# Optimization experiments

Hardware: AMD Instinct MI355X
Metric: run time of the kernel (lower is better)

## Reference

```python
import jax, jax.numpy as jnp
import numpy as np

D_MODEL = 1024
B, T = 4, 2048
NEG = -1000000000.0


def setup_inputs() -> dict:
    key = jax.random.key(0)
    kq, kk, kv = jax.random.split(key, 3)
    query = jax.random.normal(kq, (B, T, D_MODEL), dtype=jnp.float32)
    k = jax.random.normal(kk, (B, T, D_MODEL), dtype=jnp.float32)
    value = jax.random.normal(kv, (B, T, D_MODEL), dtype=jnp.float32)
    # causal mask: 1.0 where attention is disallowed (strictly upper triangular)
    mask = jnp.triu(jnp.ones((T, T), dtype=jnp.float32), k=1)
    return {"query": query, "key": k, "value": value, "mask": mask}


def reference(query, key, value, mask):
    # dk = sqrt(1/d_model); logits = QK^T / dk  (i.e. * sqrt(d_model)) -- faithful to source
    dk = jnp.sqrt(jnp.float32(1.0) / jnp.float32(D_MODEL))
    attn_logits = jnp.einsum("btc,bsc->bts", query, key) / dk
    attn_logits = attn_logits + mask * NEG  # mask broadcasts over batch
    score = jax.nn.softmax(attn_logits, axis=-1)
    attention = jnp.einsum("bts,bsc->btc", score, value)
    return attention
```

## Files before the change

kernel.cpp:

```cpp
#include <hip/hip_runtime.h>

#define BB 4
#define TT 2048
#define DD 1024
#define SCALE 32.0f
#define NTILE 136
#define L2E 1.4426950408889634f

typedef _Float16 f16;
typedef __attribute__((ext_vector_type(4))) _Float16 half4v;
typedef __attribute__((ext_vector_type(8))) _Float16 half8v;
typedef __attribute__((ext_vector_type(16))) float f32x16;

typedef const __attribute__((address_space(1))) unsigned int* gas_u32;
typedef __attribute__((address_space(3))) unsigned int* las_u32;

static __device__ inline void gload16(const void* g, void* l) {
    __builtin_amdgcn_global_load_lds((gas_u32)g, (las_u32)l, 16, 0, 0);
}

static __device__ inline half8v ld_frag(const f16* p) {
    half4v a = *(const half4v*)p;
    half4v b = *(const half4v*)(p + 4);
    half8v r;
    r[0] = a[0]; r[1] = a[1]; r[2] = a[2]; r[3] = a[3];
    r[4] = b[0]; r[5] = b[1]; r[6] = b[2]; r[7] = b[3];
    return r;
}


__global__ __launch_bounds__(256) void repack_qk(const float* __restrict__ Q,
                                                 const float* __restrict__ K,
                                                 f16* __restrict__ Qt,
                                                 f16* __restrict__ Kt) {
    __shared__ char rl[32768];
    int bid = blockIdx.x;
    int which = bid >> 10, b = (bid >> 8) & 3, mi = (bid >> 4) & 15, ks4 = bid & 15;
    const float* src = which ? K : Q;
    f16* dst = which ? Kt : Qt;
    float sc = which ? 1.0f : SCALE;

    int tid = threadIdx.x;
    int r = tid >> 1, h = tid & 1;
    const float* p = src + ((size_t)(b * TT + mi * 128 + r)) * DD + ks4 * 64 + h * 32;
#pragma unroll
    for (int j = 0; j < 4; ++j) {
        float4 x0 = *(const float4*)(p + j * 8);
        float4 x1 = *(const float4*)(p + j * 8 + 4);
        float vv[8] = {x0.x, x0.y, x0.z, x0.w, x1.x, x1.y, x1.z, x1.w};
        half8v hi, lo;
#pragma unroll
        for (int e = 0; e < 8; ++e) {
            float x = vv[e] * sc;
            f16 hh = (f16)x;
            hi[e] = hh;
            lo[e] = (f16)(x - (float)hh);
        }
        int ckl = h * 2 + (j >> 1);
        int shalf = j & 1;
        *(half8v*)(rl + ckl * 8192 + shalf * 2048 + r * 16) = hi;
        *(half8v*)(rl + ckl * 8192 + (2 + shalf) * 2048 + r * 16) = lo;
    }
    __syncthreads();
    char* gout = (char*)dst + ((size_t)((b * 16 + mi) * 64 + ks4 * 4)) * 8192 + tid * 128;
#pragma unroll
    for (int q = 0; q < 8; ++q)
        *(float4*)(gout + q * 16) = *(float4*)(rl + tid * 128 + q * 16);
}

__global__ __launch_bounds__(256) void transpose_v(const float* __restrict__ V,
                                                   f16* __restrict__ Vt) {
    __shared__ float Vs[64][129];
    int bid = blockIdx.x;
    int b = bid >> 8, kb = (bid >> 3) & 31, nj = bid & 7;
    const float* src = V + ((size_t)(b * TT + kb * 64)) * DD + nj * 128;
    int tid = threadIdx.x;
#pragma unroll
    for (int it = 0; it < 8; ++it) {
        int f4 = it * 256 + tid;
        int row = f4 >> 5, c4 = f4 & 31;
        float4 x = *(const float4*)(src + (size_t)row * DD + c4 * 4);
        Vs[row][c4 * 4 + 0] = x.x;
        Vs[row][c4 * 4 + 1] = x.y;
        Vs[row][c4 * 4 + 2] = x.z;
        Vs[row][c4 * 4 + 3] = x.w;
    }
    __syncthreads();
#pragma unroll
    for (int qq = 0; qq < 4; ++qq) {
        int q = tid * 4 + qq;
        int ckl = q >> 9, s = (q >> 7) & 3, n = q & 127;
        half8v hv;
#pragma unroll
        for (int e = 0; e < 8; ++e) hv[e] = (f16)Vs[ckl * 32 + s * 8 + e][n];
        char* out = (char*)Vt + ((size_t)((b * 8 + nj) * 64 + kb * 2 + ckl)) * 8192
                    + s * 2048 + n * 16;
        *(half8v*)out = hv;
    }
}

__global__ __launch_bounds__(256, 3) void k1_qk5(const f16* __restrict__ Qt,
                                                 const f16* __restrict__ Kt,
                                                 float* __restrict__ S) {
    __shared__ char lds[49152];

    int bid0 = blockIdx.x;
    int bid = (bid0 & 7) * (BB * NTILE / 8) + (bid0 >> 3);
    int b = bid / NTILE, rr0 = bid % NTILE;
    int mi = 0;
    while ((mi + 1) * (mi + 2) / 2 <= rr0) ++mi;
    int nj = rr0 - mi * (mi + 1) / 2;

    const char* Abase = (const char*)Qt + ((size_t)((b * 16 + mi) * 64)) * 8192;
    const char* Bbase = (const char*)Kt + ((size_t)((b * 16 + nj) * 64)) * 8192;
    float* Sb = S + (size_t)b * TT * TT + (size_t)(mi * 128) * TT + nj * 128;

    int tid = threadIdx.x;
    int lane = tid & 63;
    int wv = tid >> 6;
    int l31 = lane & 31, lhi = lane >> 5;
    int wrow = wv >> 1, wcol = wv & 1;

    int aoff[2], boff[2];
#pragma unroll
    for (int f = 0; f < 2; ++f) {
        aoff[f] = lhi * 2048 + (wrow * 64 + f * 32 + l31) * 16;
        boff[f] = lhi * 2048 + (wcol * 64 + f * 32 + l31) * 16;
    }
    int lane_go = wv * 2048 + lane * 16;
    int lane_lo = wv * 2048;

    f32x16 acc[2][2] = {};

#define K1_STAGE(CK, BUF)                                                       \
    {                                                                           \
        const char* ga = Abase + (size_t)(CK) * 8192 + lane_go;                 \
        const char* gb = Bbase + (size_t)(CK) * 8192 + lane_go;                 \
        char* la = lds + (BUF) * 16384 + lane_lo;                               \
        char* lb = la + 8192;                                                   \
        gload16(ga, la);                                                        \
        gload16(ga + 1024, la + 1024);                                          \
        gload16(gb, lb);                                                        \
        gload16(gb + 1024, lb + 1024);                                          \
    }

    K1_STAGE(0, 0);
    K1_STAGE(1, 1);
    int cb = 0;
    int sb = 2;
    for (int ck = 0; ck < 64; ++ck) {
        if (ck < 63) asm volatile("s_waitcnt vmcnt(4)" ::: "memory");
        else         asm volatile("s_waitcnt vmcnt(0)" ::: "memory");
        __builtin_amdgcn_s_barrier();
        if (ck + 2 < 64) K1_STAGE(ck + 2, sb);
        const char* As = lds + cb * 16384;
        const char* Bs = As + 8192;
        half8v ah[2], al[2], bh[2], bl[2];
#pragma unroll
        for (int f = 0; f < 2; ++f) {
            ah[f] = *(const half8v*)(As + aoff[f]);
            al[f] = *(const half8v*)(As + aoff[f] + 4096);
            bh[f] = *(const half8v*)(Bs + boff[f]);
            bl[f] = *(const half8v*)(Bs + boff[f] + 4096);
        }
#pragma unroll
        for (int fm = 0; fm < 2; ++fm)
#pragma unroll
            for (int fn = 0; fn < 2; ++fn) {
                acc[fm][fn] = __builtin_amdgcn_mfma_f32_32x32x16_f16(ah[fm], bh[fn], acc[fm][fn], 0, 0, 0);
                acc[fm][fn] = __builtin_amdgcn_mfma_f32_32x32x16_f16(ah[fm], bl[fn], acc[fm][fn], 0, 0, 0);
                acc[fm][fn] = __builtin_amdgcn_mfma_f32_32x32x16_f16(al[fm], bh[fn], acc[fm][fn], 0, 0, 0);
            }
        cb = (cb == 2) ? 0 : cb + 1;
        sb = (sb == 2) ? 0 : sb + 1;
    }
#undef K1_STAGE
#pragma unroll
    for (int fm = 0; fm < 2; ++fm)
#pragma unroll
        for (int fn = 0; fn < 2; ++fn)
#pragma unroll
            for (int g = 0; g < 16; ++g) {
                int rr = (g & 3) + 8 * (g >> 2) + 4 * lhi;
                int row = wrow * 64 + fm * 32 + rr;
                int col = wcol * 64 + fn * 32 + l31;
                Sb[(size_t)row * TT + col] = acc[fm][fn][g];
            }
}

__global__ __launch_bounds__(256) void k1b3(const float* __restrict__ S,
                                            f16* __restrict__ Pt) {
    __shared__ float red[4];
    int rowid = blockIdx.x;
    int b = rowid >> 11, t = rowid & (TT - 1);
    const float* Sr = S + ((size_t)b * TT + t) * TT;
    int tid = threadIdx.x;
    int nv = t + 1;
    int mi = t >> 7, r = t & 127;
    int rowend = (mi + 1) << 7;
    int c = tid * 8;
    bool act = c < rowend;

    float v[8] = {0, 0, 0, 0, 0, 0, 0, 0};
    if (act) {
        float4 x0 = *(const float4*)(Sr + c);
        float4 x1 = *(const float4*)(Sr + c + 4);
        v[0] = x0.x; v[1] = x0.y; v[2] = x0.z; v[3] = x0.w;
        v[4] = x1.x; v[5] = x1.y; v[6] = x1.z; v[7] = x1.w;
    }

    float m = -3.0e38f;
    if (act) {
#pragma unroll
        for (int j = 0; j < 8; ++j)
            if (c + j < nv) m = fmaxf(m, v[j]);
    }
#pragma unroll
    for (int o = 32; o > 0; o >>= 1) m = fmaxf(m, __shfl_xor(m, o));
    if ((tid & 63) == 0) red[tid >> 6] = m;
    __syncthreads();
    m = fmaxf(fmaxf(red[0], red[1]), fmaxf(red[2], red[3]));
    __syncthreads();

    float e[8];
    float s = 0.f;
#pragma unroll
    for (int j = 0; j < 8; ++j) {
        e[j] = (act && c + j < nv) ? exp2f((v[j] - m) * L2E) : 0.0f;
        s += e[j];
    }
#pragma unroll
    for (int o = 32; o > 0; o >>= 1) s += __shfl_xor(s, o);
    if ((tid & 63) == 0) red[tid >> 6] = s;
    __syncthreads();
    s = red[0] + red[1] + red[2] + red[3];
    float inv = 1.0f / s;

    if (act) {
        half8v hv;
#pragma unroll
        for (int j = 0; j < 8; ++j) hv[j] = (f16)(e[j] * inv);
        int ck = c >> 5, sl = (c >> 3) & 3;
        char* dst = (char*)Pt + ((size_t)((b * 16 + mi) * 64 + ck)) * 8192
                    + sl * 2048 + r * 16;
        *(half8v*)dst = hv;
    }
}

__global__ __launch_bounds__(256, 3) void k2_pv5(const f16* __restrict__ Pt,
                                                 const f16* __restrict__ Vt,
                                                 float* __restrict__ O) {
    __shared__ char lds[49152];

    int bid0 = blockIdx.x;
    int bid = (bid0 & 7) * 64 + (bid0 >> 3);
    int b = bid >> 7, mi = (bid >> 3) & 15, nj = bid & 7;
    int kch = (mi + 1) * 4;

    const char* Abase = (const char*)Pt + ((size_t)((b * 16 + mi) * 64)) * 8192;
    const char* Bbase = (const char*)Vt + ((size_t)((b * 8 + nj) * 64)) * 8192;
    float* Ob = O + (size_t)b * TT * DD + (size_t)(mi * 128) * DD + nj * 128;

    int tid = threadIdx.x;
    int lane = tid & 63;
    int wv = tid >> 6;
    int l31 = lane & 31, lhi = lane >> 5;
    int wrow = wv >> 1, wcol = wv & 1;

    int arow[2], brow[2];
#pragma unroll
    for (int f = 0; f < 2; ++f) {
        arow[f] = (wrow * 64 + f * 32 + l31) * 16;
        brow[f] = (wcol * 64 + f * 32 + l31) * 16;
    }
    int lane_go = wv * 2048 + lane * 16;
    int lane_lo = wv * 2048;

    f32x16 acc[2][2] = {};

#define K2_STAGE(CK, BUF)                                                       \
    {                                                                           \
        const char* ga = Abase + (size_t)(CK) * 8192 + lane_go;                 \
        const char* gb = Bbase + (size_t)(CK) * 8192 + lane_go;                 \
        char* la = lds + (BUF) * 16384 + lane_lo;                               \
        char* lb = la + 8192;                                                   \
        gload16(ga, la);                                                        \
        gload16(ga + 1024, la + 1024);                                          \
        gload16(gb, lb);                                                        \
        gload16(gb + 1024, lb + 1024);                                          \
    }

    K2_STAGE(0, 0);
    K2_STAGE(1, 1);
    int cb = 0, sb = 2;
    for (int it = 0; it < kch; ++it) {
        if (it + 1 < kch) asm volatile("s_waitcnt vmcnt(4)" ::: "memory");
        else              asm volatile("s_waitcnt vmcnt(0)" ::: "memory");
        __builtin_amdgcn_s_barrier();
        if (it + 2 < kch) K2_STAGE(it + 2, sb);
        const char* As = lds + cb * 16384;
        const char* Bs = As + 8192;
#pragma unroll
        for (int ks = 0; ks < 2; ++ks) {
            int slot = (ks * 2 + lhi) * 2048;
            half8v a0 = *(const half8v*)(As + slot + arow[0]);
            half8v a1 = *(const half8v*)(As + slot + arow[1]);
            half8v b0 = *(const half8v*)(Bs + slot + brow[0]);
            half8v b1 = *(const half8v*)(Bs + slot + brow[1]);
            acc[0][0] = __builtin_amdgcn_mfma_f32_32x32x16_f16(a0, b0, acc[0][0], 0, 0, 0);
            acc[0][1] = __builtin_amdgcn_mfma_f32_32x32x16_f16(a0, b1, acc[0][1], 0, 0, 0);
            acc[1][0] = __builtin_amdgcn_mfma_f32_32x32x16_f16(a1, b0, acc[1][0], 0, 0, 0);
            acc[1][1] = __builtin_amdgcn_mfma_f32_32x32x16_f16(a1, b1, acc[1][1], 0, 0, 0);
        }
        cb = (cb == 2) ? 0 : cb + 1;
        sb = (sb == 2) ? 0 : sb + 1;
    }
#undef K2_STAGE
#pragma unroll
    for (int fm = 0; fm < 2; ++fm)
#pragma unroll
        for (int fn = 0; fn < 2; ++fn)
#pragma unroll
            for (int g = 0; g < 16; ++g) {
                int rr = (g & 3) + 8 * (g >> 2) + 4 * lhi;
                int row = wrow * 64 + fm * 32 + rr;
                int col = wcol * 64 + fn * 32 + l31;
                Ob[(size_t)row * DD + col] = acc[fm][fn][g];
            }
}

__global__ __launch_bounds__(256, 2) void k1_qk(const float* __restrict__ Q,
                                                const float* __restrict__ Kmat,
                                                float* __restrict__ S) {
    __shared__ f16 Ah[128][36], Al[128][36], Bh[128][36], Bl[128][36];
    int bid = blockIdx.x;
    int b = bid / NTILE, r = bid % NTILE;
    int mi = 0;
    while ((mi + 1) * (mi + 2) / 2 <= r) ++mi;
    int nj = r - mi * (mi + 1) / 2;
    const float* Qb = Q + ((size_t)b * TT + (size_t)mi * 128) * DD;
    const float* Kb = Kmat + ((size_t)b * TT + (size_t)nj * 128) * DD;
    float* Sb = S + (size_t)b * TT * TT + (size_t)(mi * 128) * TT + nj * 128;
    int tid = threadIdx.x;
    int lane = tid & 63;
    int wave = tid >> 6;
    int l31 = lane & 31, lhi = lane >> 5;
    int wrow = wave >> 1, wcol = wave & 1;
    int r0 = tid >> 1;
    int c0 = (tid & 1) * 16;
    f32x16 acc[2][2] = {};
    float4 abuf[4], bbuf[4];
#pragma unroll
    for (int j = 0; j < 4; ++j) {
        abuf[j] = *(const float4*)(Qb + (size_t)r0 * DD + c0 + 4 * j);
        bbuf[j] = *(const float4*)(Kb + (size_t)r0 * DD + c0 + 4 * j);
    }
    for (int ch = 0; ch < DD / 32; ++ch) {
        __syncthreads();
#pragma unroll
        for (int j = 0; j < 4; ++j) {
            float4 a = abuf[j], bq = bbuf[j];
            float ax[4] = {a.x * SCALE, a.y * SCALE, a.z * SCALE, a.w * SCALE};
            float bx[4] = {bq.x, bq.y, bq.z, bq.w};
            half4v ahv, alv, bhv, blv;
#pragma unroll
            for (int e = 0; e < 4; ++e) {
                f16 h = (f16)ax[e];
                ahv[e] = h;
                alv[e] = (f16)(ax[e] - (float)h);
                f16 g = (f16)bx[e];
                bhv[e] = g;
                blv[e] = (f16)(bx[e] - (float)g);
            }
            *(half4v*)&Ah[r0][c0 + 4 * j] = ahv;
            *(half4v*)&Al[r0][c0 + 4 * j] = alv;
            *(half4v*)&Bh[r0][c0 + 4 * j] = bhv;
            *(half4v*)&Bl[r0][c0 + 4 * j] = blv;
        }
        __syncthreads();
// ... 165 lines not shown
    const float* q = Q + ((size_t)b * TT + t) * DD;
    int tid = threadIdx.x;
    for (int j = tid; j < DD; j += 256) { qs[j] = q[j] * SCALE; osum[j] = 0.f; }
    __syncthreads();
    float m = -3.0e38f, l = 0.f;
    for (int s = 0; s <= t; ++s) {
        const float* kr = Kmat + ((size_t)b * TT + s) * DD;
        float part = 0.f;
#pragma unroll
        for (int j = 0; j < 4; ++j) part += qs[tid * 4 + j] * kr[tid * 4 + j];
#pragma unroll
        for (int o = 32; o > 0; o >>= 1) part += __shfl_xor(part, o);
        if ((tid & 63) == 0) red[tid >> 6] = part;
        __syncthreads();
        float dot = red[0] + red[1] + red[2] + red[3];
        float mn = fmaxf(m, dot);
        float f = exp2f((m - mn) * 1.44269504f);
        float e = exp2f((dot - mn) * 1.44269504f);
        l = l * f + e;
        const float* vr = V + ((size_t)b * TT + s) * DD;
#pragma unroll
        for (int j = 0; j < 4; ++j) {
            int c = tid * 4 + j;
            osum[c] = osum[c] * f + e * vr[c];
        }
        m = mn;
        __syncthreads();
    }
    float inv = 1.f / l;
    for (int j = tid; j < DD; j += 256) O[((size_t)b * TT + t) * DD + j] = osum[j] * inv;
}

extern "C" void kernel_launch(void* const* d_in, const int* in_sizes, int n_in,
                              void* d_out, int out_size, void* d_ws, size_t ws_size,
                              hipStream_t stream) {
    const float* Q = (const float*)d_in[0];
    const float* K = (const float*)d_in[1];
    const float* V = (const float*)d_in[2];
    float* O = (float*)d_out;

    const size_t MB = 1024 * 1024;
    const size_t QT_B = 32 * MB, KT_B = 32 * MB, VT_B = 16 * MB, S_B = 64 * MB;
    const size_t FULL = QT_B + KT_B + VT_B + S_B;

    size_t sbytes = (size_t)BB * TT * TT * 4;
    size_t pbytes = (size_t)BB * TT * TT * 2;

    if (ws_size >= FULL) {
        f16* Qt = (f16*)d_ws;
        f16* Kt = (f16*)((char*)d_ws + QT_B);
        f16* Vt = (f16*)((char*)d_ws + QT_B + KT_B);
        float* S = (float*)((char*)d_ws + QT_B + KT_B + VT_B);
        f16* Pt = (f16*)d_ws;
        hipLaunchKernelGGL(repack_qk, dim3(2048), dim3(256), 0, stream, Q, K, Qt, Kt);
        hipLaunchKernelGGL(transpose_v, dim3(1024), dim3(256), 0, stream, V, Vt);
        hipLaunchKernelGGL(k1_qk5, dim3(BB * NTILE), dim3(256), 0, stream, Qt, Kt, S);
        hipLaunchKernelGGL(k1b3, dim3(BB * TT), dim3(256), 0, stream, S, Pt);
        hipLaunchKernelGGL(k2_pv5, dim3(512), dim3(256), 0, stream, Pt, Vt, O);
    } else if (ws_size >= sbytes + pbytes) {
        float* S = (float*)d_ws;
        f16* P = (f16*)((char*)d_ws + sbytes);
        hipLaunchKernelGGL(k1_qk, dim3(BB * NTILE), dim3(256), 0, stream, Q, K, S);
        hipLaunchKernelGGL(k1b_softmax, dim3(BB * TT), dim3(256), 0, stream, S, P);
        hipLaunchKernelGGL(k2_pv, dim3(BB * 16 * 8), dim3(256), 0, stream, P, V, O);
    } else {
        hipLaunchKernelGGL(fa_fallback, dim3(BB * TT), dim3(256), 0, stream, Q, K, V, O);
    }
}
```

Before: 164.1 us.

## Use two waves per block with 64x128 per-wave tiles in QK and PV GEMMs

Both MFMA GEMM kernels now run 128 threads (2 waves) instead of 256 (4 waves). Each wave computes a 64x128 output tile instead of 64x64. One wave stages the A tile and the other the B tile through global_load_lds. This gives more MFMA work per LDS fragment load and fewer LDS reads per flop. In exchange it doubles accumulator registers, halves the waves per CU available to hide latency, and keeps the same 48KB LDS per block, which caps occupancy.

```diff
diff --git a/kernel.cpp b/kernel.cpp
--- a/kernel.cpp
+++ b/kernel.cpp
@@ -99,7 +99,7 @@
     }
 }
 
-__global__ __launch_bounds__(256, 3) void k1_qk5(const f16* __restrict__ Qt,
+__global__ __launch_bounds__(128, 2) void k1_qk6(const f16* __restrict__ Qt,
                                                  const f16* __restrict__ Kt,
                                                  float* __restrict__ S) {
     __shared__ char lds[49152];
@@ -119,54 +119,53 @@
     int lane = tid & 63;
     int wv = tid >> 6;
     int l31 = lane & 31, lhi = lane >> 5;
-    int wrow = wv >> 1, wcol = wv & 1;
-
-    int aoff[2], boff[2];
-#pragma unroll
-    for (int f = 0; f < 2; ++f) {
-        aoff[f] = lhi * 2048 + (wrow * 64 + f * 32 + l31) * 16;
-        boff[f] = lhi * 2048 + (wcol * 64 + f * 32 + l31) * 16;
-    }
-    int lane_go = wv * 2048 + lane * 16;
-    int lane_lo = wv * 2048;
-
-    f32x16 acc[2][2] = {};
+
+    int aoff[2], boff[4];
+#pragma unroll
+    for (int f = 0; f < 2; ++f)
+        aoff[f] = lhi * 2048 + (wv * 64 + f * 32 + l31) * 16;
+#pragma unroll
+    for (int n = 0; n < 4; ++n)
+        boff[n] = lhi * 2048 + (n * 32 + l31) * 16;
+
+    int lane_go = lane * 16;
+    const char* gsrcbase = wv ? Bbase : Abase;
+
+    f32x16 acc[2][4] = {};
 
 #define K1_STAGE(CK, BUF)                                                       \
     {                                                                           \
-        const char* ga = Abase + (size_t)(CK) * 8192 + lane_go;                 \
-        const char* gb = Bbase + (size_t)(CK) * 8192 + lane_go;                 \
-        char* la = lds + (BUF) * 16384 + lane_lo;                               \
-        char* lb = la + 8192;                                                   \
-        gload16(ga, la);                                                        \
-        gload16(ga + 1024, la + 1024);                                          \
-        gload16(gb, lb);                                                        \
-        gload16(gb + 1024, lb + 1024);                                          \
+        const char* gs = gsrcbase + (size_t)(CK) * 8192 + lane_go;              \
+        char* ld = lds + (BUF) * 16384 + wv * 8192;                             \
+        _Pragma("unroll") for (int i = 0; i < 8; ++i)                           \
+            gload16(gs + i * 1024, ld + i * 1024);                              \
     }
 
     K1_STAGE(0, 0);
     K1_STAGE(1, 1);
-    int cb = 0;
-    int sb = 2;
+    int cb = 0, sb = 2;
     for (int ck = 0; ck < 64; ++ck) {
-        if (ck < 63) asm volatile("s_waitcnt vmcnt(4)" ::: "memory");
+        if (ck < 63) asm volatile("s_waitcnt vmcnt(8)" ::: "memory");
         else         asm volatile("s_waitcnt vmcnt(0)" ::: "memory");
         __builtin_amdgcn_s_barrier();
         if (ck + 2 < 64) K1_STAGE(ck + 2, sb);
         const char* As = lds + cb * 16384;
         const char* Bs = As + 8192;
-        half8v ah[2], al[2], bh[2], bl[2];
+        half8v ah[2], al[2], bh[4], bl[4];
 #pragma unroll
         for (int f = 0; f < 2; ++f) {
             ah[f] = *(const half8v*)(As + aoff[f]);
             al[f] = *(const half8v*)(As + aoff[f] + 4096);
-            bh[f] = *(const half8v*)(Bs + boff[f]);
-            bl[f] = *(const half8v*)(Bs + boff[f] + 4096);
+        }
+#pragma unroll
+        for (int n = 0; n < 4; ++n) {
+            bh[n] = *(const half8v*)(Bs + boff[n]);
+            bl[n] = *(const half8v*)(Bs + boff[n] + 4096);
         }
 #pragma unroll
         for (int fm = 0; fm < 2; ++fm)
 #pragma unroll
-            for (int fn = 0; fn < 2; ++fn) {
+            for (int fn = 0; fn < 4; ++fn) {
                 acc[fm][fn] = __builtin_amdgcn_mfma_f32_32x32x16_f16(ah[fm], bh[fn], acc[fm][fn], 0, 0, 0);
                 acc[fm][fn] = __builtin_amdgcn_mfma_f32_32x32x16_f16(ah[fm], bl[fn], acc[fm][fn], 0, 0, 0);
                 acc[fm][fn] = __builtin_amdgcn_mfma_f32_32x32x16_f16(al[fm], bh[fn], acc[fm][fn], 0, 0, 0);
@@ -178,12 +177,12 @@
 #pragma unroll
     for (int fm = 0; fm < 2; ++fm)
 #pragma unroll
-        for (int fn = 0; fn < 2; ++fn)
+        for (int fn = 0; fn < 4; ++fn)
 #pragma unroll
             for (int g = 0; g < 16; ++g) {
                 int rr = (g & 3) + 8 * (g >> 2) + 4 * lhi;
-                int row = wrow * 64 + fm * 32 + rr;
-                int col = wcol * 64 + fn * 32 + l31;
+                int row = wv * 64 + fm * 32 + rr;
+                int col = fn * 32 + l31;
                 Sb[(size_t)row * TT + col] = acc[fm][fn][g];
             }
 }
@@ -247,7 +246,7 @@
     }
 }
 
-__global__ __launch_bounds__(256, 3) void k2_pv5(const f16* __restrict__ Pt,
+__global__ __launch_bounds__(128, 2) void k2_pv6(const f16* __restrict__ Pt,
                                                  const f16* __restrict__ Vt,
                                                  float* __restrict__ O) {
     __shared__ char lds[49152];
@@ -265,36 +264,31 @@
     int lane = tid & 63;
     int wv = tid >> 6;
     int l31 = lane & 31, lhi = lane >> 5;
-    int wrow = wv >> 1, wcol = wv & 1;
-
-    int arow[2], brow[2];
-#pragma unroll
-    for (int f = 0; f < 2; ++f) {
-        arow[f] = (wrow * 64 + f * 32 + l31) * 16;
-        brow[f] = (wcol * 64 + f * 32 + l31) * 16;
-    }
-    int lane_go = wv * 2048 + lane * 16;
-    int lane_lo = wv * 2048;
-
-    f32x16 acc[2][2] = {};
+
+    int arow[2], brow[4];
+#pragma unroll
+    for (int f = 0; f < 2; ++f) arow[f] = (wv * 64 + f * 32 + l31) * 16;
+#pragma unroll
+    for (int n = 0; n < 4; ++n) brow[n] = (n * 32 + l31) * 16;
+
+    int lane_go = lane * 16;
+    const char* gsrcbase = wv ? Bbase : Abase;
+
+    f32x16 acc[2][4] = {};
 
 #define K2_STAGE(CK, BUF)                                                       \
     {                                                                           \
-        const char* ga = Abase + (size_t)(CK) * 8192 + lane_go;                 \
-        const char* gb = Bbase + (size_t)(CK) * 8192 + lane_go;                 \
-        char* la = lds + (BUF) * 16384 + lane_lo;                               \
-        char* lb = la + 8192;                                                   \
-        gload16(ga, la);                                                        \
-        gload16(ga + 1024, la + 1024);                                          \
-        gload16(gb, lb);                                                        \
-        gload16(gb + 1024, lb + 1024);                                          \
+        const char* gs = gsrcbase + (size_t)(CK) * 8192 + lane_go;              \
+        char* ld = lds + (BUF) * 16384 + wv * 8192;                             \
+        _Pragma("unroll") for (int i = 0; i < 8; ++i)                           \
+            gload16(gs + i * 1024, ld + i * 1024);                              \
     }
 
     K2_STAGE(0, 0);
     K2_STAGE(1, 1);
     int cb = 0, sb = 2;
     for (int it = 0; it < kch; ++it) {
-        if (it + 1 < kch) asm volatile("s_waitcnt vmcnt(4)" ::: "memory");
+        if (it + 1 < kch) asm volatile("s_waitcnt vmcnt(8)" ::: "memory");
         else              asm volatile("s_waitcnt vmcnt(0)" ::: "memory");
         __builtin_amdgcn_s_barrier();
         if (it + 2 < kch) K2_STAGE(it + 2, sb);
@@ -307,10 +301,16 @@
             half8v a1 = *(const half8v*)(As + slot + arow[1]);
             half8v b0 = *(const half8v*)(Bs + slot + brow[0]);
             half8v b1 = *(const half8v*)(Bs + slot + brow[1]);
+            half8v b2 = *(const half8v*)(Bs + slot + brow[2]);
+            half8v b3 = *(const half8v*)(Bs + slot + brow[3]);
             acc[0][0] = __builtin_amdgcn_mfma_f32_32x32x16_f16(a0, b0, acc[0][0], 0, 0, 0);
             acc[0][1] = __builtin_amdgcn_mfma_f32_32x32x16_f16(a0, b1, acc[0][1], 0, 0, 0);
+            acc[0][2] = __builtin_amdgcn_mfma_f32_32x32x16_f16(a0, b2, acc[0][2], 0, 0, 0);
+            acc[0][3] = __builtin_amdgcn_mfma_f32_32x32x16_f16(a0, b3, acc[0][3], 0, 0, 0);
             acc[1][0] = __builtin_amdgcn_mfma_f32_32x32x16_f16(a1, b0, acc[1][0], 0, 0, 0);
             acc[1][1] = __builtin_amdgcn_mfma_f32_32x32x16_f16(a1, b1, acc[1][1], 0, 0, 0);
+            acc[1][2] = __builtin_amdgcn_mfma_f32_32x32x16_f16(a1, b2, acc[1][2], 0, 0, 0);
+            acc[1][3] = __builtin_amdgcn_mfma_f32_32x32x16_f16(a1, b3, acc[1][3], 0, 0, 0);
         }
         cb = (cb == 2) ? 0 : cb + 1;
         sb = (sb == 2) ? 0 : sb + 1;
@@ -319,12 +319,12 @@
 #pragma unroll
     for (int fm = 0; fm < 2; ++fm)
 #pragma unroll
-        for (int fn = 0; fn < 2; ++fn)
+        for (int fn = 0; fn < 4; ++fn)
 #pragma unroll
             for (int g = 0; g < 16; ++g) {
                 int rr = (g & 3) + 8 * (g >> 2) + 4 * lhi;
-                int row = wrow * 64 + fm * 32 + rr;
-                int col = wcol * 64 + fn * 32 + l31;
+                int row = wv * 64 + fm * 32 + rr;
+                int col = fn * 32 + l31;
                 Ob[(size_t)row * DD + col] = acc[fm][fn][g];
             }
 }
@@ -598,9 +598,9 @@
         f16* Pt = (f16*)d_ws;
         hipLaunchKernelGGL(repack_qk, dim3(2048), dim3(256), 0, stream, Q, K, Qt, Kt);
         hipLaunchKernelGGL(transpose_v, dim3(1024), dim3(256), 0, stream, V, Vt);
-        hipLaunchKernelGGL(k1_qk5, dim3(BB * NTILE), dim3(256), 0, stream, Qt, Kt, S);
+        hipLaunchKernelGGL(k1_qk6, dim3(BB * NTILE), dim3(128), 0, stream, Qt, Kt, S);
         hipLaunchKernelGGL(k1b3, dim3(BB * TT), dim3(256), 0, stream, S, Pt);
-        hipLaunchKernelGGL(k2_pv5, dim3(512), dim3(256), 0, stream, Pt, Vt, O);
+        hipLaunchKernelGGL(k2_pv6, dim3(512), dim3(128), 0, stream, Pt, Vt, O);
     } else if (ws_size >= sbytes + pbytes) {
         float* S = (float*)d_ws;
         f16* P = (f16*)((char*)d_ws + sbytes);
```

New measurement: 179.1 us. 1.09x slower.

## Merge Q/K/V prep kernels and halve QK/PV tiles to 64x128 for more blocks

Applied to the files above, without the earlier changes.

Merges the Q/K repack and the V transpose into one prep kernel to save a launch. The QK^T and PV GEMM kernels now use 64x128 output tiles computed by 2 waves of 128 threads, with a new mapping over the causal tiles, instead of 128x128 tiles on 4 waves. This doubles the grid (1088 and 1024 blocks versus 544 and 512) for better CU coverage and finer causal load balance. In exchange, each K/V tile is loaded from memory twice as often, MFMA work per byte loaded is lower, and the LDS footprint per block changes.

```diff
diff --git a/kernel.cpp b/kernel.cpp
--- a/kernel.cpp
+++ b/kernel.cpp
@@ -29,137 +29,149 @@
 }
 
 
-__global__ __launch_bounds__(256) void repack_qk(const float* __restrict__ Q,
-                                                 const float* __restrict__ K,
-                                                 f16* __restrict__ Qt,
-                                                 f16* __restrict__ Kt) {
-    __shared__ char rl[32768];
+__global__ __launch_bounds__(256) void prep(const float* __restrict__ Q,
+                                            const float* __restrict__ K,
+                                            const float* __restrict__ V,
+                                            f16* __restrict__ Qt,
+                                            f16* __restrict__ Kt,
+                                            f16* __restrict__ Vt) {
+    __shared__ char plds[33024];
     int bid = blockIdx.x;
-    int which = bid >> 10, b = (bid >> 8) & 3, mi = (bid >> 4) & 15, ks4 = bid & 15;
-    const float* src = which ? K : Q;
-    f16* dst = which ? Kt : Qt;
-    float sc = which ? 1.0f : SCALE;
-
-    int tid = threadIdx.x;
-    int r = tid >> 1, h = tid & 1;
-    const float* p = src + ((size_t)(b * TT + mi * 128 + r)) * DD + ks4 * 64 + h * 32;
-#pragma unroll
-    for (int j = 0; j < 4; ++j) {
-        float4 x0 = *(const float4*)(p + j * 8);
-        float4 x1 = *(const float4*)(p + j * 8 + 4);
-        float vv[8] = {x0.x, x0.y, x0.z, x0.w, x1.x, x1.y, x1.z, x1.w};
-        half8v hi, lo;
-#pragma unroll
-        for (int e = 0; e < 8; ++e) {
-            float x = vv[e] * sc;
-            f16 hh = (f16)x;
-            hi[e] = hh;
-            lo[e] = (f16)(x - (float)hh);
-        }
-        int ckl = h * 2 + (j >> 1);
-        int shalf = j & 1;
-        *(half8v*)(rl + ckl * 8192 + shalf * 2048 + r * 16) = hi;
-        *(half8v*)(rl + ckl * 8192 + (2 + shalf) * 2048 + r * 16) = lo;
-    }
-    __syncthreads();
-    char* gout = (char*)dst + ((size_t)((b * 16 + mi) * 64 + ks4 * 4)) * 8192 + tid * 128;
-#pragma unroll
-    for (int q = 0; q < 8; ++q)
-        *(float4*)(gout + q * 16) = *(float4*)(rl + tid * 128 + q * 16);
-}
-
-__global__ __launch_bounds__(256) void transpose_v(const float* __restrict__ V,
-                                                   f16* __restrict__ Vt) {
-    __shared__ float Vs[64][129];
-    int bid = blockIdx.x;
-    int b = bid >> 8, kb = (bid >> 3) & 31, nj = bid & 7;
-    const float* src = V + ((size_t)(b * TT + kb * 64)) * DD + nj * 128;
-    int tid = threadIdx.x;
-#pragma unroll
-    for (int it = 0; it < 8; ++it) {
-        int f4 = it * 256 + tid;
-        int row = f4 >> 5, c4 = f4 & 31;
-        float4 x = *(const float4*)(src + (size_t)row * DD + c4 * 4);
-        Vs[row][c4 * 4 + 0] = x.x;
-        Vs[row][c4 * 4 + 1] = x.y;
-        Vs[row][c4 * 4 + 2] = x.z;
-        Vs[row][c4 * 4 + 3] = x.w;
-    }
-    __syncthreads();
-#pragma unroll
-    for (int qq = 0; qq < 4; ++qq) {
-        int q = tid * 4 + qq;
-        int ckl = q >> 9, s = (q >> 7) & 3, n = q & 127;
-        half8v hv;
-#pragma unroll
-        for (int e = 0; e < 8; ++e) hv[e] = (f16)Vs[ckl * 32 + s * 8 + e][n];
-        char* out = (char*)Vt + ((size_t)((b * 8 + nj) * 64 + kb * 2 + ckl)) * 8192
-                    + s * 2048 + n * 16;
-        *(half8v*)out = hv;
-    }
-}
-
-__global__ __launch_bounds__(256, 3) void k1_qk5(const f16* __restrict__ Qt,
+    int tid = threadIdx.x;
+    if (bid < 2048) {
+        char* rl = plds;
+        int which = bid >> 10, b = (bid >> 8) & 3, mi = (bid >> 4) & 15, ks4 = bid & 15;
+        const float* src = which ? K : Q;
+        f16* dst = which ? Kt : Qt;
+        float sc = which ? 1.0f : SCALE;
+        int r = tid >> 1, h = tid & 1;
+        const float* p = src + ((size_t)(b * TT + mi * 128 + r)) * DD + ks4 * 64 + h * 32;
+#pragma unroll
+        for (int j = 0; j < 4; ++j) {
+            float4 x0 = *(const float4*)(p + j * 8);
+            float4 x1 = *(const float4*)(p + j * 8 + 4);
+            float vv[8] = {x0.x, x0.y, x0.z, x0.w, x1.x, x1.y, x1.z, x1.w};
+            half8v hi, lo;
+#pragma unroll
+            for (int e = 0; e < 8; ++e) {
+                float x = vv[e] * sc;
+                f16 hh = (f16)x;
+                hi[e] = hh;
+                lo[e] = (f16)(x - (float)hh);
+            }
+            int ckl = h * 2 + (j >> 1);
+            int shalf = j & 1;
+            *(half8v*)(rl + ckl * 8192 + shalf * 2048 + r * 16) = hi;
+            *(half8v*)(rl + ckl * 8192 + (2 + shalf) * 2048 + r * 16) = lo;
+        }
+        __syncthreads();
+        char* gout = (char*)dst + ((size_t)((b * 16 + mi) * 64 + ks4 * 4)) * 8192 + tid * 128;
+#pragma unroll
+        for (int q = 0; q < 8; ++q)
+            *(float4*)(gout + q * 16) = *(float4*)(rl + tid * 128 + q * 16);
+    } else {
+        float (*Vs)[129] = (float(*)[129])plds;
+        int bid2 = bid - 2048;
+        int b = bid2 >> 8, kb = (bid2 >> 3) & 31, nj = bid2 & 7;
+        const float* src = V + ((size_t)(b * TT + kb * 64)) * DD + nj * 128;
+#pragma unroll
+        for (int it = 0; it < 8; ++it) {
+            int f4 = it * 256 + tid;
+            int row = f4 >> 5, c4 = f4 & 31;
+            float4 x = *(const float4*)(src + (size_t)row * DD + c4 * 4);
+            Vs[row][c4 * 4 + 0] = x.x;
+            Vs[row][c4 * 4 + 1] = x.y;
+            Vs[row][c4 * 4 + 2] = x.z;
+            Vs[row][c4 * 4 + 3] = x.w;
+        }
+        __syncthreads();
+#pragma unroll
+        for (int qq = 0; qq < 4; ++qq) {
+            int q = tid * 4 + qq;
+            int ckl = q >> 9, s = (q >> 7) & 3, n = q & 127;
+            half8v hv;
+#pragma unroll
+            for (int e = 0; e < 8; ++e) hv[e] = (f16)Vs[ckl * 32 + s * 8 + e][n];
+            char* out = (char*)Vt + ((size_t)((b * 8 + nj) * 64 + kb * 2 + ckl)) * 8192
+                        + s * 2048 + n * 16;
+            *(half8v*)out = hv;
+        }
+    }
+}
+
+__global__ __launch_bounds__(128, 2) void k1_qk7(const f16* __restrict__ Qt,
                                                  const f16* __restrict__ Kt,
                                                  float* __restrict__ S) {
-    __shared__ char lds[49152];
+    __shared__ char lds[36864];
 
     int bid0 = blockIdx.x;
-    int bid = (bid0 & 7) * (BB * NTILE / 8) + (bid0 >> 3);
-    int b = bid / NTILE, rr0 = bid % NTILE;
-    int mi = 0;
-    while ((mi + 1) * (mi + 2) / 2 <= rr0) ++mi;
-    int nj = rr0 - mi * (mi + 1) / 2;
-
-    const char* Abase = (const char*)Qt + ((size_t)((b * 16 + mi) * 64)) * 8192;
+    int bid = (bid0 & 7) * 136 + (bid0 >> 3);
+    int b = bid / 272, r = bid % 272;
+    int p = 0;
+    while ((p + 1) * (p + 2) <= r) ++p;
+    int rem = r - p * (p + 1);
+    int second = (rem >= p + 1);
+    int mi2 = 2 * p + second;
+    int nj = second ? rem - (p + 1) : rem;
+    int mi = mi2 >> 1, rhalf = mi2 & 1;
+
+    const char* Abase = (const char*)Qt + ((size_t)((b * 16 + mi) * 64)) * 8192
+                        + rhalf * 1024;
     const char* Bbase = (const char*)Kt + ((size_t)((b * 16 + nj) * 64)) * 8192;
-    float* Sb = S + (size_t)b * TT * TT + (size_t)(mi * 128) * TT + nj * 128;
+    float* Sb = S + (size_t)b * TT * TT + (size_t)(mi2 * 64) * TT + nj * 128;
 
     int tid = threadIdx.x;
     int lane = tid & 63;
     int wv = tid >> 6;
     int l31 = lane & 31, lhi = lane >> 5;
-    int wrow = wv >> 1, wcol = wv & 1;
 
     int aoff[2], boff[2];
 #pragma unroll
     for (int f = 0; f < 2; ++f) {
-        aoff[f] = lhi * 2048 + (wrow * 64 + f * 32 + l31) * 16;
-        boff[f] = lhi * 2048 + (wcol * 64 + f * 32 + l31) * 16;
-    }
-    int lane_go = wv * 2048 + lane * 16;
-    int lane_lo = wv * 2048;
+        aoff[f] = lhi * 1024 + (f * 32 + l31) * 16;
+        boff[f] = lhi * 2048 + (wv * 64 + f * 32 + l31) * 16;
+    }
+    int lane16 = lane * 16;
 
     f32x16 acc[2][2] = {};
 
 #define K1_STAGE(CK, BUF)                                                       \
     {                                                                           \
-        const char* ga = Abase + (size_t)(CK) * 8192 + lane_go;                 \
-        const char* gb = Bbase + (size_t)(CK) * 8192 + lane_go;                 \
-        char* la = lds + (BUF) * 16384 + lane_lo;                               \
-        char* lb = la + 8192;                                                   \
-        gload16(ga, la);                                                        \
-        gload16(ga + 1024, la + 1024);                                          \
-        gload16(gb, lb);                                                        \
-        gload16(gb + 1024, lb + 1024);                                          \
+        const char* ga = Abase + (size_t)(CK) * 8192 + lane16;                  \
+        const char* gb = Bbase + (size_t)(CK) * 8192 + lane16;                  \
+        char* l0 = lds + (BUF) * 12288;                                         \
+        if (wv == 0) {                                                          \
+            gload16(ga, l0);                                                    \
+            gload16(ga + 2048, l0 + 1024);                                      \
+            gload16(ga + 4096, l0 + 2048);                                      \
+            gload16(ga + 6144, l0 + 3072);                                      \
+            gload16(gb, l0 + 4096);                                             \
+            gload16(gb + 1024, l0 + 5120);                                      \
+        } else {                                                                \
+            gload16(gb + 2048, l0 + 6144);                                      \
+            gload16(gb + 3072, l0 + 7168);                                      \
+            gload16(gb + 4096, l0 + 8192);                                      \
+            gload16(gb + 5120, l0 + 9216);                                      \
+            gload16(gb + 6144, l0 + 10240);                                     \
+            gload16(gb + 7168, l0 + 11264);                                     \
+        }                                                                       \
     }
 
     K1_STAGE(0, 0);
     K1_STAGE(1, 1);
-    int cb = 0;
-    int sb = 2;
+    int cb = 0, sb = 2;
     for (int ck = 0; ck < 64; ++ck) {
-        if (ck < 63) asm volatile("s_waitcnt vmcnt(4)" ::: "memory");
+        if (ck < 63) asm volatile("s_waitcnt vmcnt(6)" ::: "memory");
         else         asm volatile("s_waitcnt vmcnt(0)" ::: "memory");
         __builtin_amdgcn_s_barrier();
         if (ck + 2 < 64) K1_STAGE(ck + 2, sb);
-        const char* As = lds + cb * 16384;
-        const char* Bs = As + 8192;
+        const char* As = lds + cb * 12288;
+        const char* Bs = As + 4096;
         half8v ah[2], al[2], bh[2], bl[2];
 #pragma unroll
         for (int f = 0; f < 2; ++f) {
             ah[f] = *(const half8v*)(As + aoff[f]);
-            al[f] = *(const half8v*)(As + aoff[f] + 4096);
+            al[f] = *(const half8v*)(As + aoff[f] + 2048);
             bh[f] = *(const half8v*)(Bs + boff[f]);
             bl[f] = *(const half8v*)(Bs + boff[f] + 4096);
         }
@@ -182,8 +194,8 @@
 #pragma unroll
             for (int g = 0; g < 16; ++g) {
                 int rr = (g & 3) + 8 * (g >> 2) + 4 * lhi;
-                int row = wrow * 64 + fm * 32 + rr;
-                int col = wcol * 64 + fn * 32 + l31;
+                int row = fm * 32 + rr;
+                int col = wv * 64 + fn * 32 + l31;
                 Sb[(size_t)row * TT + col] = acc[fm][fn][g];
             }
 }
@@ -247,66 +259,77 @@
     }
 }
 
-__global__ __launch_bounds__(256, 3) void k2_pv5(const f16* __restrict__ Pt,
+__global__ __launch_bounds__(128, 2) void k2_pv7(const f16* __restrict__ Pt,
                                                  const f16* __restrict__ Vt,
                                                  float* __restrict__ O) {
-    __shared__ char lds[49152];
+    __shared__ char lds[36864];
 
     int bid0 = blockIdx.x;
-    int bid = (bid0 & 7) * 64 + (bid0 >> 3);
-    int b = bid >> 7, mi = (bid >> 3) & 15, nj = bid & 7;
-    int kch = (mi + 1) * 4;
-
-    const char* Abase = (const char*)Pt + ((size_t)((b * 16 + mi) * 64)) * 8192;
+    int bid = (bid0 & 7) * 128 + (bid0 >> 3);
+    int b = bid >> 8, r = (bid >> 3) & 31, nj = bid & 7;
+    int kch = 2 * r + 2;
+    int mi = r >> 1, rhalf = r & 1;
+
+    const char* Abase = (const char*)Pt + ((size_t)((b * 16 + mi) * 64)) * 8192
+                        + rhalf * 1024;
     const char* Bbase = (const char*)Vt + ((size_t)((b * 8 + nj) * 64)) * 8192;
-    float* Ob = O + (size_t)b * TT * DD + (size_t)(mi * 128) * DD + nj * 128;
+    float* Ob = O + (size_t)b * TT * DD + (size_t)(r * 64) * DD + nj * 128;
 
     int tid = threadIdx.x;
     int lane = tid & 63;
     int wv = tid >> 6;
     int l31 = lane & 31, lhi = lane >> 5;
-    int wrow = wv >> 1, wcol = wv & 1;
+    int lane16 = lane * 16;
 
     int arow[2], brow[2];
 #pragma unroll
     for (int f = 0; f < 2; ++f) {
-        arow[f] = (wrow * 64 + f * 32 + l31) * 16;
-        brow[f] = (wcol * 64 + f * 32 + l31) * 16;
-    }
-    int lane_go = wv * 2048 + lane * 16;
-    int lane_lo = wv * 2048;
+        arow[f] = (f * 32 + l31) * 16;
+        brow[f] = (wv * 64 + f * 32 + l31) * 16;
+    }
 
     f32x16 acc[2][2] = {};
 
 #define K2_STAGE(CK, BUF)                                                       \
     {                                                                           \
-        const char* ga = Abase + (size_t)(CK) * 8192 + lane_go;                 \
-        const char* gb = Bbase + (size_t)(CK) * 8192 + lane_go;                 \
-        char* la = lds + (BUF) * 16384 + lane_lo;                               \
-        char* lb = la + 8192;                                                   \
-        gload16(ga, la);                                                        \
-        gload16(ga + 1024, la + 1024);                                          \
-        gload16(gb, lb);                                                        \
-        gload16(gb + 1024, lb + 1024);                                          \
+        const char* ga = Abase + (size_t)(CK) * 8192 + lane16;                  \
+        const char* gb = Bbase + (size_t)(CK) * 8192 + lane16;                  \
+        char* l0 = lds + (BUF) * 12288;                                         \
+        if (wv == 0) {                                                          \
+            gload16(ga, l0);                                                    \
+            gload16(ga + 2048, l0 + 1024);                                      \
+            gload16(ga + 4096, l0 + 2048);                                      \
+            gload16(ga + 6144, l0 + 3072);                                      \
+            gload16(gb, l0 + 4096);                                             \
+            gload16(gb + 1024, l0 + 5120);                                      \
+        } else {                                                                \
+            gload16(gb + 2048, l0 + 6144);                                      \
+            gload16(gb + 3072, l0 + 7168);                                      \
+            gload16(gb + 4096, l0 + 8192);                                      \
+            gload16(gb + 5120, l0 + 9216);                                      \
+            gload16(gb + 6144, l0 + 10240);                                     \
+            gload16(gb + 7168, l0 + 11264);                                     \
+        }                                                                       \
     }
 
     K2_STAGE(0, 0);
     K2_STAGE(1, 1);
     int cb = 0, sb = 2;
     for (int it = 0; it < kch; ++it) {
-        if (it + 1 < kch) asm volatile("s_waitcnt vmcnt(4)" ::: "memory");
+        if (it + 1 < kch) asm volatile("s_waitcnt vmcnt(6)" ::: "memory");
         else              asm volatile("s_waitcnt vmcnt(0)" ::: "memory");
         __builtin_amdgcn_s_barrier();
         if (it + 2 < kch) K2_STAGE(it + 2, sb);
-        const char* As = lds + cb * 16384;
-        const char* Bs = As + 8192;
+        const char* As = lds + cb * 12288;
+        const char* Bs = As + 4096;
 #pragma unroll
         for (int ks = 0; ks < 2; ++ks) {
-            int slot = (ks * 2 + lhi) * 2048;
-            half8v a0 = *(const half8v*)(As + slot + arow[0]);
-            half8v a1 = *(const half8v*)(As + slot + arow[1]);
-            half8v b0 = *(const half8v*)(Bs + slot + brow[0]);
-            half8v b1 = *(const half8v*)(Bs + slot + brow[1]);
+            int asl = (ks * 2 + lhi) * 1024;
+            int bsl = (ks * 2 + lhi) * 2048;
+            half8v a0 = *(const half8v*)(As + asl + arow[0]);
+            half8v a1 = *(const half8v*)(As + asl + arow[1]);
+            half8v b0 = *(const half8v*)(Bs + bsl + brow[0]);
+            half8v b1 = *(const half8v*)(Bs + bsl + brow[1]);
             acc[0][0] = __builtin_amdgcn_mfma_f32_32x32x16_f16(a0, b0, acc[0][0], 0, 0, 0);
             acc[0][1] = __builtin_amdgcn_mfma_f32_32x32x16_f16(a0, b1, acc[0][1], 0, 0, 0);
             acc[1][0] = __builtin_amdgcn_mfma_f32_32x32x16_f16(a1, b0, acc[1][0], 0, 0, 0);
@@ -323,8 +346,8 @@
 #pragma unroll
             for (int g = 0; g < 16; ++g) {
                 int rr = (g & 3) + 8 * (g >> 2) + 4 * lhi;
-                int row = wrow * 64 + fm * 32 + rr;
-                int col = wcol * 64 + fn * 32 + l31;
+                int row = fm * 32 + rr;
+                int col = wv * 64 + fn * 32 + l31;
                 Ob[(size_t)row * DD + col] = acc[fm][fn][g];
             }
 }
@@ -596,11 +619,10 @@
         f16* Vt = (f16*)((char*)d_ws + QT_B + KT_B);
         float* S = (float*)((char*)d_ws + QT_B + KT_B + VT_B);
         f16* Pt = (f16*)d_ws;
-        hipLaunchKernelGGL(repack_qk, dim3(2048), dim3(256), 0, stream, Q, K, Qt, Kt);
-        hipLaunchKernelGGL(transpose_v, dim3(1024), dim3(256), 0, stream, V, Vt);
-        hipLaunchKernelGGL(k1_qk5, dim3(BB * NTILE), dim3(256), 0, stream, Qt, Kt, S);
+        hipLaunchKernelGGL(prep, dim3(3072), dim3(256), 0, stream, Q, K, V, Qt, Kt, Vt);
+        hipLaunchKernelGGL(k1_qk7, dim3(1088), dim3(128), 0, stream, Qt, Kt, S);
         hipLaunchKernelGGL(k1b3, dim3(BB * TT), dim3(256), 0, stream, S, Pt);
-        hipLaunchKernelGGL(k2_pv5, dim3(512), dim3(256), 0, stream, Pt, Vt, O);
+        hipLaunchKernelGGL(k2_pv7, dim3(1024), dim3(128), 0, stream, Pt, Vt, O);
     } else if (ws_size >= sbytes + pbytes) {
         float* S = (float*)d_ws;
         f16* P = (f16*)((char*)d_ws + sbytes);
```

Measured after the change: 175.4 us. +6.9%, slower.

## Merge prep kernels and switch QK and PV GEMMs to double-buffered staging

Applied to the files above, without the earlier changes.

Folds the Q/K repack and the V transpose into a single `prep` launch, dispatching on block index, to save one kernel launch. The QK kernel drops from a three-stage LDS ring with explicit `vmcnt` waits to a two-buffer scheme synchronised by `__syncthreads`, shrinking LDS to 32 KB. The PV kernel now stages two K-chunks per iteration into 64 KB of double-buffered LDS, which halves the iteration count and the number of barriers, with occupancy lowered to 2. The trade is shallower prefetch: each load now has only one compute step to hide behind, which can expose more memory latency.

```diff
diff --git a/kernel.cpp b/kernel.cpp
--- a/kernel.cpp
+++ b/kernel.cpp
@@ -29,80 +29,80 @@
 }
 
 
-__global__ __launch_bounds__(256) void repack_qk(const float* __restrict__ Q,
-                                                 const float* __restrict__ K,
-                                                 f16* __restrict__ Qt,
-                                                 f16* __restrict__ Kt) {
-    __shared__ char rl[32768];
+__global__ __launch_bounds__(256) void prep(const float* __restrict__ Q,
+                                            const float* __restrict__ K,
+                                            const float* __restrict__ V,
+                                            f16* __restrict__ Qt,
+                                            f16* __restrict__ Kt,
+                                            f16* __restrict__ Vt) {
+    __shared__ char plds[33024];
     int bid = blockIdx.x;
-    int which = bid >> 10, b = (bid >> 8) & 3, mi = (bid >> 4) & 15, ks4 = bid & 15;
-    const float* src = which ? K : Q;
-    f16* dst = which ? Kt : Qt;
-    float sc = which ? 1.0f : SCALE;
-
-    int tid = threadIdx.x;
-    int r = tid >> 1, h = tid & 1;
-    const float* p = src + ((size_t)(b * TT + mi * 128 + r)) * DD + ks4 * 64 + h * 32;
-#pragma unroll
-    for (int j = 0; j < 4; ++j) {
-        float4 x0 = *(const float4*)(p + j * 8);
-        float4 x1 = *(const float4*)(p + j * 8 + 4);
-        float vv[8] = {x0.x, x0.y, x0.z, x0.w, x1.x, x1.y, x1.z, x1.w};
-        half8v hi, lo;
-#pragma unroll
-        for (int e = 0; e < 8; ++e) {
-            float x = vv[e] * sc;
-            f16 hh = (f16)x;
-            hi[e] = hh;
-            lo[e] = (f16)(x - (float)hh);
-        }
-        int ckl = h * 2 + (j >> 1);
-        int shalf = j & 1;
-        *(half8v*)(rl + ckl * 8192 + shalf * 2048 + r * 16) = hi;
-        *(half8v*)(rl + ckl * 8192 + (2 + shalf) * 2048 + r * 16) = lo;
-    }
-    __syncthreads();
-    char* gout = (char*)dst + ((size_t)((b * 16 + mi) * 64 + ks4 * 4)) * 8192 + tid * 128;
-#pragma unroll
-    for (int q = 0; q < 8; ++q)
-        *(float4*)(gout + q * 16) = *(float4*)(rl + tid * 128 + q * 16);
-}
-
-__global__ __launch_bounds__(256) void transpose_v(const float* __restrict__ V,
-                                                   f16* __restrict__ Vt) {
-    __shared__ float Vs[64][129];
-    int bid = blockIdx.x;
-    int b = bid >> 8, kb = (bid >> 3) & 31, nj = bid & 7;
-    const float* src = V + ((size_t)(b * TT + kb * 64)) * DD + nj * 128;
-    int tid = threadIdx.x;
-#pragma unroll
-    for (int it = 0; it < 8; ++it) {
-        int f4 = it * 256 + tid;
-        int row = f4 >> 5, c4 = f4 & 31;
-        float4 x = *(const float4*)(src + (size_t)row * DD + c4 * 4);
-        Vs[row][c4 * 4 + 0] = x.x;
-        Vs[row][c4 * 4 + 1] = x.y;
-        Vs[row][c4 * 4 + 2] = x.z;
-        Vs[row][c4 * 4 + 3] = x.w;
-    }
-    __syncthreads();
-#pragma unroll
-    for (int qq = 0; qq < 4; ++qq) {
-        int q = tid * 4 + qq;
-        int ckl = q >> 9, s = (q >> 7) & 3, n = q & 127;
-        half8v hv;
-#pragma unroll
-        for (int e = 0; e < 8; ++e) hv[e] = (f16)Vs[ckl * 32 + s * 8 + e][n];
-        char* out = (char*)Vt + ((size_t)((b * 8 + nj) * 64 + kb * 2 + ckl)) * 8192
-                    + s * 2048 + n * 16;
-        *(half8v*)out = hv;
-    }
-}
-
-__global__ __launch_bounds__(256, 3) void k1_qk5(const f16* __restrict__ Qt,
+    int tid = threadIdx.x;
+    if (bid < 2048) {
+        char* rl = plds;
+        int which = bid >> 10, b = (bid >> 8) & 3, mi = (bid >> 4) & 15, ks4 = bid & 15;
+        const float* src = which ? K : Q;
+        f16* dst = which ? Kt : Qt;
+        float sc = which ? 1.0f : SCALE;
+        int r = tid >> 1, h = tid & 1;
+        const float* p = src + ((size_t)(b * TT + mi * 128 + r)) * DD + ks4 * 64 + h * 32;
+#pragma unroll
+        for (int j = 0; j < 4; ++j) {
+            float4 x0 = *(const float4*)(p + j * 8);
+            float4 x1 = *(const float4*)(p + j * 8 + 4);
+            float vv[8] = {x0.x, x0.y, x0.z, x0.w, x1.x, x1.y, x1.z, x1.w};
+            half8v hi, lo;
+#pragma unroll
+            for (int e = 0; e < 8; ++e) {
+                float x = vv[e] * sc;
+                f16 hh = (f16)x;
+                hi[e] = hh;
+                lo[e] = (f16)(x - (float)hh);
+            }
+            int ckl = h * 2 + (j >> 1);
+            int shalf = j & 1;
+            *(half8v*)(rl + ckl * 8192 + shalf * 2048 + r * 16) = hi;
+            *(half8v*)(rl + ckl * 8192 + (2 + shalf) * 2048 + r * 16) = lo;
+        }
+        __syncthreads();
+        char* gout = (char*)dst + ((size_t)((b * 16 + mi) * 64 + ks4 * 4)) * 8192 + tid * 128;
+#pragma unroll
+        for (int q = 0; q < 8; ++q)
+            *(float4*)(gout + q * 16) = *(float4*)(rl + tid * 128 + q * 16);
+    } else {
+        float (*Vs)[129] = (float(*)[129])plds;
+        int bid2 = bid - 2048;
+        int b = bid2 >> 8, kb = (bid2 >> 3) & 31, nj = bid2 & 7;
+        const float* src = V + ((size_t)(b * TT + kb * 64)) * DD + nj * 128;
+#pragma unroll
+        for (int it = 0; it < 8; ++it) {
+            int f4 = it * 256 + tid;
+            int row = f4 >> 5, c4 = f4 & 31;
+            float4 x = *(const float4*)(src + (size_t)row * DD + c4 * 4);
+            Vs[row][c4 * 4 + 0] = x.x;
+            Vs[row][c4 * 4 + 1] = x.y;
+            Vs[row][c4 * 4 + 2] = x.z;
+            Vs[row][c4 * 4 + 3] = x.w;
+        }
+        __syncthreads();
+#pragma unroll
+        for (int qq = 0; qq < 4; ++qq) {
+            int q = tid * 4 + qq;
+            int ckl = q >> 9, s = (q >> 7) & 3, n = q & 127;
+            half8v hv;
+#pragma unroll
+            for (int e = 0; e < 8; ++e) hv[e] = (f16)Vs[ckl * 32 + s * 8 + e][n];
+            char* out = (char*)Vt + ((size_t)((b * 8 + nj) * 64 + kb * 2 + ckl)) * 8192
+                        + s * 2048 + n * 16;
+            *(half8v*)out = hv;
+        }
+    }
+}
+
+__global__ __launch_bounds__(256, 3) void k1_qk3(const f16* __restrict__ Qt,
                                                  const f16* __restrict__ Kt,
                                                  float* __restrict__ S) {
-    __shared__ char lds[49152];
+    __shared__ char lds[32768];
 
     int bid0 = blockIdx.x;
     int bid = (bid0 & 7) * (BB * NTILE / 8) + (bid0 >> 3);
@@ -124,8 +124,10 @@
     int aoff[2], boff[2];
 #pragma unroll
     for (int f = 0; f < 2; ++f) {
-        aoff[f] = lhi * 2048 + (wrow * 64 + f * 32 + l31) * 16;
-        boff[f] = lhi * 2048 + (wcol * 64 + f * 32 + l31) * 16;
+        int ra = wrow * 64 + f * 32 + l31;
+        int rb = wcol * 64 + f * 32 + l31;
+        aoff[f] = lhi * 2048 + ra * 16;
+        boff[f] = lhi * 2048 + rb * 16;
     }
     int lane_go = wv * 2048 + lane * 16;
     int lane_lo = wv * 2048;
@@ -145,15 +147,11 @@
     }
 
     K1_STAGE(0, 0);
-    K1_STAGE(1, 1);
-    int cb = 0;
-    int sb = 2;
+    int cur = 0;
     for (int ck = 0; ck < 64; ++ck) {
-        if (ck < 63) asm volatile("s_waitcnt vmcnt(4)" ::: "memory");
-        else         asm volatile("s_waitcnt vmcnt(0)" ::: "memory");
-        __builtin_amdgcn_s_barrier();
-        if (ck + 2 < 64) K1_STAGE(ck + 2, sb);
-        const char* As = lds + cb * 16384;
+        __syncthreads();
+        if (ck + 1 < 64) K1_STAGE(ck + 1, cur ^ 1);
+        const char* As = lds + cur * 16384;
         const char* Bs = As + 8192;
         half8v ah[2], al[2], bh[2], bl[2];
 #pragma unroll
@@ -171,8 +169,7 @@
                 acc[fm][fn] = __builtin_amdgcn_mfma_f32_32x32x16_f16(ah[fm], bl[fn], acc[fm][fn], 0, 0, 0);
                 acc[fm][fn] = __builtin_amdgcn_mfma_f32_32x32x16_f16(al[fm], bh[fn], acc[fm][fn], 0, 0, 0);
             }
-        cb = (cb == 2) ? 0 : cb + 1;
-        sb = (sb == 2) ? 0 : sb + 1;
+        cur ^= 1;
     }
 #undef K1_STAGE
 #pragma unroll
@@ -247,15 +244,15 @@
     }
 }
 
-__global__ __launch_bounds__(256, 3) void k2_pv5(const f16* __restrict__ Pt,
+__global__ __launch_bounds__(256, 2) void k2_pv8(const f16* __restrict__ Pt,
                                                  const f16* __restrict__ Vt,
                                                  float* __restrict__ O) {
-    __shared__ char lds[49152];
+    __shared__ char lds[65536];
 
     int bid0 = blockIdx.x;
     int bid = (bid0 & 7) * 64 + (bid0 >> 3);
     int b = bid >> 7, mi = (bid >> 3) & 15, nj = bid & 7;
-    int kch = (mi + 1) * 4;
+    int kch = 2 * (mi + 1);
 
     const char* Abase = (const char*)Pt + ((size_t)((b * 16 + mi) * 64)) * 8192;
     const char* Bbase = (const char*)Vt + ((size_t)((b * 8 + nj) * 64)) * 8192;
@@ -266,6 +263,7 @@
     int wv = tid >> 6;
     int l31 = lane & 31, lhi = lane >> 5;
     int wrow = wv >> 1, wcol = wv & 1;
+    int lane16 = lane * 16;
 
     int arow[2], brow[2];
 #pragma unroll
@@ -273,47 +271,45 @@
         arow[f] = (wrow * 64 + f * 32 + l31) * 16;
         brow[f] = (wcol * 64 + f * 32 + l31) * 16;
     }
-    int lane_go = wv * 2048 + lane * 16;
-    int lane_lo = wv * 2048;
 
     f32x16 acc[2][2] = {};
 
 #define K2_STAGE(CK, BUF)                                                       \
     {                                                                           \
-        const char* ga = Abase + (size_t)(CK) * 8192 + lane_go;                 \
-        const char* gb = Bbase + (size_t)(CK) * 8192 + lane_go;                 \
-        char* la = lds + (BUF) * 16384 + lane_lo;                               \
-        char* lb = la + 8192;                                                   \
+        const char* ga = Abase + (size_t)(CK) * 16384 + wv * 4096 + lane16;     \
+        const char* gb = Bbase + (size_t)(CK) * 16384 + wv * 4096 + lane16;     \
+        char* la = lds + (BUF) * 32768 + wv * 4096;                             \
+        char* lb = la + 16384;                                                  \
         gload16(ga, la);                                                        \
         gload16(ga + 1024, la + 1024);                                          \
+        gload16(ga + 2048, la + 2048);                                          \
+        gload16(ga + 3072, la + 3072);                                          \
         gload16(gb, lb);                                                        \
         gload16(gb + 1024, lb + 1024);                                          \
+        gload16(gb + 2048, lb + 2048);                                          \
+        gload16(gb + 3072, lb + 3072);                                          \
     }
 
     K2_STAGE(0, 0);
-    K2_STAGE(1, 1);
-    int cb = 0, sb = 2;
+    int cur = 0;
     for (int it = 0; it < kch; ++it) {
-        if (it + 1 < kch) asm volatile("s_waitcnt vmcnt(4)" ::: "memory");
-        else              asm volatile("s_waitcnt vmcnt(0)" ::: "memory");
-        __builtin_amdgcn_s_barrier();
-        if (it + 2 < kch) K2_STAGE(it + 2, sb);
-        const char* As = lds + cb * 16384;
-        const char* Bs = As + 8192;
-#pragma unroll
-        for (int ks = 0; ks < 2; ++ks) {
-            int slot = (ks * 2 + lhi) * 2048;
-            half8v a0 = *(const half8v*)(As + slot + arow[0]);
-            half8v a1 = *(const half8v*)(As + slot + arow[1]);
-            half8v b0 = *(const half8v*)(Bs + slot + brow[0]);
-            half8v b1 = *(const half8v*)(Bs + slot + brow[1]);
+        __syncthreads();
+        if (it + 1 < kch) K2_STAGE(it + 1, cur ^ 1);
+        const char* As = lds + cur * 32768;
+        const char* Bs = As + 16384;
+#pragma unroll
+        for (int j = 0; j < 4; ++j) {
+            int slotbase = (j >> 1) * 8192 + ((j & 1) * 2 + lhi) * 2048;
+            half8v a0 = *(const half8v*)(As + slotbase + arow[0]);
+            half8v a1 = *(const half8v*)(As + slotbase + arow[1]);
+            half8v b0 = *(const half8v*)(Bs + slotbase + brow[0]);
+            half8v b1 = *(const half8v*)(Bs + slotbase + brow[1]);
             acc[0][0] = __builtin_amdgcn_mfma_f32_32x32x16_f16(a0, b0, acc[0][0], 0, 0, 0);
             acc[0][1] = __builtin_amdgcn_mfma_f32_32x32x16_f16(a0, b1, acc[0][1], 0, 0, 0);
             acc[1][0] = __builtin_amdgcn_mfma_f32_32x32x16_f16(a1, b0, acc[1][0], 0, 0, 0);
             acc[1][1] = __builtin_amdgcn_mfma_f32_32x32x16_f16(a1, b1, acc[1][1], 0, 0, 0);
         }
-        cb = (cb == 2) ? 0 : cb + 1;
-        sb = (sb == 2) ? 0 : sb + 1;
+        cur ^= 1;
     }
 #undef K2_STAGE
 #pragma unroll
@@ -596,11 +592,10 @@
         f16* Vt = (f16*)((char*)d_ws + QT_B + KT_B);
         float* S = (float*)((char*)d_ws + QT_B + KT_B + VT_B);
         f16* Pt = (f16*)d_ws;
-        hipLaunchKernelGGL(repack_qk, dim3(2048), dim3(256), 0, stream, Q, K, Qt, Kt);
-        hipLaunchKernelGGL(transpose_v, dim3(1024), dim3(256), 0, stream, V, Vt);
-        hipLaunchKernelGGL(k1_qk5, dim3(BB * NTILE), dim3(256), 0, stream, Qt, Kt, S);
+        hipLaunchKernelGGL(prep, dim3(3072), dim3(256), 0, stream, Q, K, V, Qt, Kt, Vt);
+        hipLaunchKernelGGL(k1_qk3, dim3(BB * NTILE), dim3(256), 0, stream, Qt, Kt, S);
         hipLaunchKernelGGL(k1b3, dim3(BB * TT), dim3(256), 0, stream, S, Pt);
-        hipLaunchKernelGGL(k2_pv5, dim3(512), dim3(256), 0, stream, Pt, Vt, O);
+        hipLaunchKernelGGL(k2_pv8, dim3(512), dim3(256), 0, stream, Pt, Vt, O);
     } else if (ws_size >= sbytes + pbytes) {
         float* S = (float*)d_ws;
         f16* P = (f16*)((char*)d_ws + sbytes);
```

Measured after the change: 160.7 us (median of 2 runs). 2.0% less time.
